# Performance work log

Hardware: AMD Instinct MI355X
Metric: run time of the kernel (lower is better)

## Reference

```python
import jax, jax.numpy as jnp
import numpy as np

N_OSC = 60
B = 65536
DT = 0.1
STEPS = 10
PHI_INV = 2.0 / (1.0 + np.sqrt(5.0))


def setup_inputs() -> dict:
    key = jax.random.key(0)
    k1, k2, k3 = jax.random.split(key, 3)
    theta = jax.random.uniform(k1, (B, N_OSC), dtype=jnp.float32) * (2.0 * np.pi) - np.pi
    K = jax.random.normal(k2, (N_OSC, N_OSC), dtype=jnp.float32) * 0.1
    omega = jax.random.normal(k3, (N_OSC,), dtype=jnp.float32) * 0.1
    return {
        'theta': theta,
        'K': K,
        'omega': omega,
        'K_global': jnp.float32(PHI_INV),
        'coupling_mod': jnp.float32(0.6),        # phase_coupling['quasi_crystal']
        'neg_entropy_gate': jnp.float32(0.5),
        'critical_slow_factor': jnp.float32(0.1),
        'delta_s_neg': jnp.float32(0.8),          # NegativeEntropyState constant
        'relaxation_time': jnp.float32(5.0),      # NegativeEntropyState constant
    }


def reference(theta, K, omega, K_global, coupling_mod, neg_entropy_gate,
              critical_slow_factor, delta_s_neg, relaxation_time):
    n = theta.shape[-1]
    K_eff = K * coupling_mod                               # [n, n]
    critical_factor = 1.0 / (1.0 + critical_slow_factor * relaxation_time)
    eff_dt = DT * critical_factor
    boost = 1.0 + neg_entropy_gate * delta_s_neg
    scale = K_global * boost / n

    def step(th, _):
        # theta_diff[b, i, j] = th[b, j] - th[b, i]
        diff = th[..., None, :] - th[..., :, None]          # [B, n, n]
        coupling_sum = jnp.sum(K_eff * jnp.sin(diff), axis=-1)  # [B, n]
        th = th + eff_dt * (omega + scale * coupling_sum)
        th = jnp.arctan2(jnp.sin(th), jnp.cos(th))          # wrap to (-pi, pi]
        return th, None

    theta, _ = jax.lax.scan(step, theta, None, length=STEPS)
    cos_m = jnp.cos(theta).mean(axis=-1)
    sin_m = jnp.sin(theta).mean(axis=-1)
    coherence = jnp.sqrt(cos_m ** 2 + sin_m ** 2)           # [B]
    return theta, coherence
```

## Files before the change

kernel.cpp:

```cpp
#include <hip/hip_runtime.h>
#include <stdint.h>
#include <math.h>


#define B_TOTAL 65536
#define NOSC 60
#define STEPS 10

using short8  = __attribute__((ext_vector_type(8))) short;
using floatx4 = __attribute__((ext_vector_type(4))) float;

#if __has_builtin(__builtin_amdgcn_perm)
__device__ __forceinline__ unsigned int perm_b32(unsigned int s0, unsigned int s1, unsigned int sel) {
    return __builtin_amdgcn_perm(s0, s1, sel);
}
#else
__device__ __forceinline__ unsigned int perm_b32(unsigned int s0, unsigned int s1, unsigned int sel) {
    unsigned long long pool = ((unsigned long long)s0 << 32) | s1;
    unsigned int r = 0;
#pragma unroll
    for (int b = 0; b < 4; ++b) {
        unsigned int s = (sel >> (8 * b)) & 0xff;
        r |= ((unsigned int)((pool >> (8 * s)) & 0xff)) << (8 * b);
    }
    return r;
}
#endif

__device__ __forceinline__ unsigned int fbits(float x)   { return __builtin_bit_cast(unsigned int, x); }
__device__ __forceinline__ float        bitsf(unsigned int u) { return __builtin_bit_cast(float, u); }

__global__ __launch_bounds__(64, 2)
void kuramoto_kernel(const float* __restrict__ theta_in,
                     const float* __restrict__ Kmat,
                     const float* __restrict__ omega,
                     const float* __restrict__ p_kglobal,
                     const float* __restrict__ p_cmod,
                     const float* __restrict__ p_gate,
                     const float* __restrict__ p_slow,
                     const float* __restrict__ p_dsneg,
                     const float* __restrict__ p_relax,
                     float* __restrict__ theta_out,
                     float* __restrict__ coh_out)
{
    __shared__ uint64_t tile[16 * 66];

    const int lane = threadIdx.x & 63;
    const int lidx = lane & 15;
    const int quad = lane >> 4;

    const float kglobal = p_kglobal[0];
    const float cmod    = p_cmod[0];
    const float gate    = p_gate[0];
    const float slow    = p_slow[0];
    const float dsneg   = p_dsneg[0];
    const float relax   = p_relax[0];

    float eff_dt, scale;
    {
#pragma clang fp contract(off)
        const float a     = slow * relax;
        const float b     = 1.0f + a;
        const float crit  = 1.0f / b;
        eff_dt            = 0.1f * crit;
        const float boost = 1.0f + gate * dsneg;
        scale             = (kglobal * boost) / 60.0f;
    }

    const int batch0 = blockIdx.x * 16;

    short8 KH[4][2], KL[4][2];
#pragma unroll
    for (int nt = 0; nt < 4; ++nt) {
        const int n = nt * 16 + lidx;
        const bool okn = (n < NOSC);
#pragma unroll
        for (int kt = 0; kt < 2; ++kt) {
            const int k0 = kt * 32 + quad * 8;
            float kv[8];
            if (okn && (k0 + 7) < NOSC) {
                const float4* rp = (const float4*)(Kmat + n * NOSC + k0);
                const float4 a = rp[0], b = rp[1];
                kv[0]=a.x; kv[1]=a.y; kv[2]=a.z; kv[3]=a.w;
                kv[4]=b.x; kv[5]=b.y; kv[6]=b.z; kv[7]=b.w;
            } else {
#pragma unroll
                for (int j = 0; j < 8; ++j)
                    kv[j] = (okn && (k0 + j) < NOSC) ? Kmat[n * NOSC + k0 + j] : 0.0f;
            }
#pragma unroll
            for (int j = 0; j < 8; ++j) {
                const float v = kv[j] * cmod;
                const unsigned int hb = fbits(v) & 0xffff0000u;
                const float rlo = v - bitsf(hb);
                KH[nt][kt][j] = (short)(hb >> 16);
                KL[nt][kt][j] = (short)(fbits(rlo) >> 16);
            }
        }
    }

    float th[4][4], sn[4][4], cn[4][4];
    float omg[4];
#pragma unroll
    for (int nt = 0; nt < 4; ++nt) {
        const int i = nt * 16 + lidx;
        omg[nt] = (i < NOSC) ? omega[i] : 0.0f;
#pragma unroll
        for (int r = 0; r < 4; ++r) {
            const int b = batch0 + quad * 4 + r;
            th[nt][r] = (i < NOSC) ? theta_in[b * NOSC + i] : 0.0f;
            __sincosf(th[nt][r], &sn[nt][r], &cn[nt][r]);
        }
    }

    const float PI_F = 3.14159274101257324f;
    const float C_HI = 6.28318548202514648f;
    const float C_LO = -1.7484556e-7f;

    for (int t = 0; t < STEPS; ++t) {
#pragma unroll
        for (int nt = 0; nt < 4; ++nt) {
#pragma unroll
            for (int r = 0; r < 4; ++r) {
                const float s = sn[nt][r], c = cn[nt][r];
                const unsigned int us = fbits(s);
                const float rs = s - bitsf(us & 0xffff0000u);
                const unsigned int uc = fbits(c);
                const float rc = c - bitsf(uc & 0xffff0000u);
                const unsigned int w0 = perm_b32(fbits(rs), us, 0x07060302u);
                const unsigned int w1 = perm_b32(fbits(rc), uc, 0x07060302u);
                tile[(quad * 4 + r) * 66 + nt * 16 + lidx] =
                    (uint64_t)w0 | ((uint64_t)w1 << 32);
            }
        }
        __syncthreads();

        floatx4 accS[4], accC[4];
#pragma unroll
        for (int nt = 0; nt < 4; ++nt) { accS[nt] = (floatx4)0.0f; accC[nt] = (floatx4)0.0f; }
#pragma unroll
        for (int kt = 0; kt < 2; ++kt) {
            const uint4* p = (const uint4*)(tile + lidx * 66 + kt * 32 + quad * 8);
            uint4 q[4];
            q[0] = p[0]; q[1] = p[1]; q[2] = p[2]; q[3] = p[3];
            union U { short8 v; unsigned int u[4]; };
            U ash, asl, ach, acl;
#pragma unroll
            for (int pr = 0; pr < 4; ++pr) {
                ash.u[pr] = perm_b32(q[pr].z, q[pr].x, 0x05040100u);
                asl.u[pr] = perm_b32(q[pr].z, q[pr].x, 0x07060302u);
                ach.u[pr] = perm_b32(q[pr].w, q[pr].y, 0x05040100u);
                acl.u[pr] = perm_b32(q[pr].w, q[pr].y, 0x07060302u);
            }
#pragma unroll
            for (int nt = 0; nt < 4; ++nt) {
                accS[nt] = __builtin_amdgcn_mfma_f32_16x16x32_bf16(ash.v, KH[nt][kt], accS[nt], 0, 0, 0);
                accS[nt] = __builtin_amdgcn_mfma_f32_16x16x32_bf16(asl.v, KH[nt][kt], accS[nt], 0, 0, 0);
                accS[nt] = __builtin_amdgcn_mfma_f32_16x16x32_bf16(ash.v, KL[nt][kt], accS[nt], 0, 0, 0);
                accC[nt] = __builtin_amdgcn_mfma_f32_16x16x32_bf16(ach.v, KH[nt][kt], accC[nt], 0, 0, 0);
                accC[nt] = __builtin_amdgcn_mfma_f32_16x16x32_bf16(acl.v, KH[nt][kt], accC[nt], 0, 0, 0);
                accC[nt] = __builtin_amdgcn_mfma_f32_16x16x32_bf16(ach.v, KL[nt][kt], accC[nt], 0, 0, 0);
            }
        }

#pragma unroll
        for (int nt = 0; nt < 4; ++nt) {
#pragma unroll
            for (int r = 0; r < 4; ++r) {
                const float S = accS[nt][r];
                const float C = accC[nt][r];
                const float coup = cn[nt][r] * S - sn[nt][r] * C;
                float nth;
                {
#pragma clang fp contract(off)
                    const float t1 = scale * coup;
                    const float t2 = omg[nt] + t1;
                    const float t3 = eff_dt * t2;
                    nth = th[nt][r] + t3;
                }
                float n = 0.0f;
                n = (nth >=  PI_F) ?  1.0f : n;
                n = (nth <= -PI_F) ? -1.0f : n;
                float y = fmaf(n, -C_HI, nth);
                y = fmaf(n, -C_LO, y);
                th[nt][r] = y;
                __sincosf(y, &sn[nt][r], &cn[nt][r]);
            }
        }
    }

#pragma unroll
    for (int nt = 0; nt < 4; ++nt) {
        const int i = nt * 16 + lidx;
        if (i < NOSC) {
#pragma unroll
            for (int r = 0; r < 4; ++r) {
                const int b = batch0 + quad * 4 + r;
                theta_out[b * NOSC + i] = th[nt][r];
            }
        }
    }

    float pc[4], ps[4];
#pragma unroll
    for (int r = 0; r < 4; ++r) { pc[r] = 0.0f; ps[r] = 0.0f; }
#pragma unroll
    for (int nt = 0; nt < 4; ++nt) {
        const int i = nt * 16 + lidx;
        const bool ok = (i < NOSC);
#pragma unroll
        for (int r = 0; r < 4; ++r) {
            pc[r] += ok ? cn[nt][r] : 0.0f;
            ps[r] += ok ? sn[nt][r] : 0.0f;
        }
    }
#pragma unroll
    for (int mask = 1; mask < 16; mask <<= 1) {
#pragma unroll
        for (int r = 0; r < 4; ++r) {
            pc[r] += __shfl_xor(pc[r], mask, 16);
            ps[r] += __shfl_xor(ps[r], mask, 16);
        }
    }
    if (lidx == 0) {
#pragma unroll
        for (int r = 0; r < 4; ++r) {
            const float cm = pc[r] / 60.0f;
            const float sm = ps[r] / 60.0f;
            coh_out[batch0 + quad * 4 + r] = sqrtf(cm * cm + sm * sm);
        }
    }
}

extern "C" void kernel_launch(void* const* d_in, const int* in_sizes, int n_in,
                              void* d_out, int out_size, void* d_ws, size_t ws_size,
                              hipStream_t stream) {
    const float* theta = (const float*)d_in[0];
    const float* Kmat  = (const float*)d_in[1];
    const float* omg   = (const float*)d_in[2];
    const float* kg    = (const float*)d_in[3];
    const float* cmod  = (const float*)d_in[4];
    const float* gate  = (const float*)d_in[5];
    const float* slow  = (const float*)d_in[6];
    const float* dsn   = (const float*)d_in[7];
    const float* relax = (const float*)d_in[8];
    float* out = (float*)d_out;

    kuramoto_kernel<<<dim3(B_TOTAL / 16), dim3(64), 0, stream>>>(
        theta, Kmat, omg, kg, cmod, gate, slow, dsn, relax,
        out, out + (size_t)B_TOTAL * NOSC);
}
```

Measured before the change: 123.3 us.

## Transpose MFMA formulation to keep phase state in registers, removing LDS staging

```diff
diff --git a/kernel.cpp b/kernel.cpp
--- a/kernel.cpp
+++ b/kernel.cpp
@@ -7,7 +7,7 @@
 #define NOSC 60
 #define STEPS 10
 
-using short8  = __attribute__((ext_vector_type(8))) short;
+using short4v = __attribute__((ext_vector_type(4))) short;
 using floatx4 = __attribute__((ext_vector_type(4))) float;
 
 #if __has_builtin(__builtin_amdgcn_perm)
@@ -27,8 +27,23 @@
 }
 #endif
 
-__device__ __forceinline__ unsigned int fbits(float x)   { return __builtin_bit_cast(unsigned int, x); }
+__device__ __forceinline__ unsigned int fbits(float x)        { return __builtin_bit_cast(unsigned int, x); }
 __device__ __forceinline__ float        bitsf(unsigned int u) { return __builtin_bit_cast(float, u); }
+
+#if __has_builtin(__builtin_amdgcn_mfma_f32_16x16x16bf16_1k)
+__device__ __forceinline__ floatx4 mfma16(short4v a, short4v b, floatx4 c) {
+    return __builtin_amdgcn_mfma_f32_16x16x16bf16_1k(a, b, c, 0, 0, 0);
+}
+#else
+__device__ __forceinline__ floatx4 mfma16(short4v a, short4v b, floatx4 c) {
+    asm("v_mfma_f32_16x16x16_bf16 %0, %1, %2, %0" : "+v"(c) : "v"(a), "v"(b));
+    return c;
+}
+#endif
+
+__device__ __forceinline__ unsigned int pack_hi_pair(float a, float b) {
+    return perm_b32(fbits(b), fbits(a), 0x07060302u);
+}
 
 __global__ __launch_bounds__(64, 2)
 void kuramoto_kernel(const float* __restrict__ theta_in,
@@ -43,8 +58,6 @@
                      float* __restrict__ theta_out,
                      float* __restrict__ coh_out)
 {
-    __shared__ uint64_t tile[16 * 66];
-
     const int lane = threadIdx.x & 63;
     const int lidx = lane & 15;
     const int quad = lane >> 4;
@@ -68,49 +81,55 @@
     }
 
     const int batch0 = blockIdx.x * 16;
-
-    short8 KH[4][2], KL[4][2];
-#pragma unroll
-    for (int nt = 0; nt < 4; ++nt) {
-        const int n = nt * 16 + lidx;
-        const bool okn = (n < NOSC);
-#pragma unroll
-        for (int kt = 0; kt < 2; ++kt) {
-            const int k0 = kt * 32 + quad * 8;
-            float kv[8];
-            if (okn && (k0 + 7) < NOSC) {
-                const float4* rp = (const float4*)(Kmat + n * NOSC + k0);
-                const float4 a = rp[0], b = rp[1];
-                kv[0]=a.x; kv[1]=a.y; kv[2]=a.z; kv[3]=a.w;
-                kv[4]=b.x; kv[5]=b.y; kv[6]=b.z; kv[7]=b.w;
+    const int brow   = (batch0 + lidx) * NOSC;
+
+    short4v AH[4][4], AL[4][4];
+#pragma unroll
+    for (int nt = 0; nt < 4; ++nt) {
+        const int i = nt * 16 + lidx;
+        const bool okn = (i < NOSC);
+#pragma unroll
+        for (int kt = 0; kt < 4; ++kt) {
+            const int k0 = kt * 16 + quad * 4;
+            float kv[4];
+            if (okn && (k0 + 3) < NOSC) {
+                const float4 a = *(const float4*)(Kmat + i * NOSC + k0);
+                kv[0] = a.x; kv[1] = a.y; kv[2] = a.z; kv[3] = a.w;
             } else {
 #pragma unroll
-                for (int j = 0; j < 8; ++j)
-                    kv[j] = (okn && (k0 + j) < NOSC) ? Kmat[n * NOSC + k0 + j] : 0.0f;
-            }
-#pragma unroll
-            for (int j = 0; j < 8; ++j) {
+                for (int j = 0; j < 4; ++j)
+                    kv[j] = (okn && (k0 + j) < NOSC) ? Kmat[i * NOSC + k0 + j] : 0.0f;
+            }
+            short4v h, l;
+#pragma unroll
+            for (int j = 0; j < 4; ++j) {
                 const float v = kv[j] * cmod;
                 const unsigned int hb = fbits(v) & 0xffff0000u;
                 const float rlo = v - bitsf(hb);
-                KH[nt][kt][j] = (short)(hb >> 16);
-                KL[nt][kt][j] = (short)(fbits(rlo) >> 16);
-            }
-        }
-    }
-
-    float th[4][4], sn[4][4], cn[4][4];
-    float omg[4];
-#pragma unroll
-    for (int nt = 0; nt < 4; ++nt) {
-        const int i = nt * 16 + lidx;
-        omg[nt] = (i < NOSC) ? omega[i] : 0.0f;
-#pragma unroll
-        for (int r = 0; r < 4; ++r) {
-            const int b = batch0 + quad * 4 + r;
-            th[nt][r] = (i < NOSC) ? theta_in[b * NOSC + i] : 0.0f;
+                h[j] = (short)(hb >> 16);
+                l[j] = (short)(fbits(rlo) >> 16);
+            }
+            AH[nt][kt] = h;
+            AL[nt][kt] = l;
+        }
+    }
+
+    float th[4][4], sn[4][4], cn[4][4], omg[4][4];
+#pragma unroll
+    for (int nt = 0; nt < 4; ++nt) {
+        const int o0 = nt * 16 + quad * 4;
+        if (o0 + 3 < NOSC) {
+            const float4 tv = *(const float4*)(theta_in + brow + o0);
+            const float4 ov = *(const float4*)(omega + o0);
+            th[nt][0] = tv.x; th[nt][1] = tv.y; th[nt][2] = tv.z; th[nt][3] = tv.w;
+            omg[nt][0] = ov.x; omg[nt][1] = ov.y; omg[nt][2] = ov.z; omg[nt][3] = ov.w;
+        } else {
+#pragma unroll
+            for (int r = 0; r < 4; ++r) { th[nt][r] = 0.0f; omg[nt][r] = 0.0f; }
+        }
+#pragma unroll
+        for (int r = 0; r < 4; ++r)
             __sincosf(th[nt][r], &sn[nt][r], &cn[nt][r]);
-        }
     }
 
     const float PI_F = 3.14159274101257324f;
@@ -118,48 +137,39 @@
     const float C_LO = -1.7484556e-7f;
 
     for (int t = 0; t < STEPS; ++t) {
-#pragma unroll
-        for (int nt = 0; nt < 4; ++nt) {
+        floatx4 accS[4], accC[4];
+#pragma unroll
+        for (int nt = 0; nt < 4; ++nt) { accS[nt] = (floatx4)0.0f; accC[nt] = (floatx4)0.0f; }
+
+#pragma unroll
+        for (int kt = 0; kt < 4; ++kt) {
+            union PU { unsigned int u[2]; short4v v; };
+            PU bsh, bsl, bch, bcl;
+            float sl[4], cl[4];
 #pragma unroll
             for (int r = 0; r < 4; ++r) {
-                const float s = sn[nt][r], c = cn[nt][r];
-                const unsigned int us = fbits(s);
-                const float rs = s - bitsf(us & 0xffff0000u);
-                const unsigned int uc = fbits(c);
-                const float rc = c - bitsf(uc & 0xffff0000u);
-                const unsigned int w0 = perm_b32(fbits(rs), us, 0x07060302u);
-                const unsigned int w1 = perm_b32(fbits(rc), uc, 0x07060302u);
-                tile[(quad * 4 + r) * 66 + nt * 16 + lidx] =
-                    (uint64_t)w0 | ((uint64_t)w1 << 32);
-            }
-        }
-        __syncthreads();
-
-        floatx4 accS[4], accC[4];
-#pragma unroll
-        for (int nt = 0; nt < 4; ++nt) { accS[nt] = (floatx4)0.0f; accC[nt] = (floatx4)0.0f; }
-#pragma unroll
-        for (int kt = 0; kt < 2; ++kt) {
-            const uint4* p = (const uint4*)(tile + lidx * 66 + kt * 32 + quad * 8);
-            uint4 q[4];
-            q[0] = p[0]; q[1] = p[1]; q[2] = p[2]; q[3] = p[3];
-            union U { short8 v; unsigned int u[4]; };
-            U ash, asl, ach, acl;
-#pragma unroll
-            for (int pr = 0; pr < 4; ++pr) {
-                ash.u[pr] = perm_b32(q[pr].z, q[pr].x, 0x05040100u);
-                asl.u[pr] = perm_b32(q[pr].z, q[pr].x, 0x07060302u);
-                ach.u[pr] = perm_b32(q[pr].w, q[pr].y, 0x05040100u);
-                acl.u[pr] = perm_b32(q[pr].w, q[pr].y, 0x07060302u);
-            }
+                const unsigned int us = fbits(sn[kt][r]);
+                sl[r] = sn[kt][r] - bitsf(us & 0xffff0000u);
+                const unsigned int uc = fbits(cn[kt][r]);
+                cl[r] = cn[kt][r] - bitsf(uc & 0xffff0000u);
+            }
+            bsh.u[0] = pack_hi_pair(sn[kt][0], sn[kt][1]);
+            bsh.u[1] = pack_hi_pair(sn[kt][2], sn[kt][3]);
+            bsl.u[0] = pack_hi_pair(sl[0], sl[1]);
+            bsl.u[1] = pack_hi_pair(sl[2], sl[3]);
+            bch.u[0] = pack_hi_pair(cn[kt][0], cn[kt][1]);
+            bch.u[1] = pack_hi_pair(cn[kt][2], cn[kt][3]);
+            bcl.u[0] = pack_hi_pair(cl[0], cl[1]);
+            bcl.u[1] = pack_hi_pair(cl[2], cl[3]);
+
 #pragma unroll
             for (int nt = 0; nt < 4; ++nt) {
-                accS[nt] = __builtin_amdgcn_mfma_f32_16x16x32_bf16(ash.v, KH[nt][kt], accS[nt], 0, 0, 0);
-                accS[nt] = __builtin_amdgcn_mfma_f32_16x16x32_bf16(asl.v, KH[nt][kt], accS[nt], 0, 0, 0);
-                accS[nt] = __builtin_amdgcn_mfma_f32_16x16x32_bf16(ash.v, KL[nt][kt], accS[nt], 0, 0, 0);
-                accC[nt] = __builtin_amdgcn_mfma_f32_16x16x32_bf16(ach.v, KH[nt][kt], accC[nt], 0, 0, 0);
-                accC[nt] = __builtin_amdgcn_mfma_f32_16x16x32_bf16(acl.v, KH[nt][kt], accC[nt], 0, 0, 0);
-                accC[nt] = __builtin_amdgcn_mfma_f32_16x16x32_bf16(ach.v, KL[nt][kt], accC[nt], 0, 0, 0);
+                accS[nt] = mfma16(AH[nt][kt], bsh.v, accS[nt]);
+                accS[nt] = mfma16(AL[nt][kt], bsh.v, accS[nt]);
+                accS[nt] = mfma16(AH[nt][kt], bsl.v, accS[nt]);
+                accC[nt] = mfma16(AH[nt][kt], bch.v, accC[nt]);
+                accC[nt] = mfma16(AL[nt][kt], bch.v, accC[nt]);
+                accC[nt] = mfma16(AH[nt][kt], bcl.v, accC[nt]);
             }
         }
 
@@ -174,7 +184,7 @@
                 {
 #pragma clang fp contract(off)
                     const float t1 = scale * coup;
-                    const float t2 = omg[nt] + t1;
+                    const float t2 = omg[nt][r] + t1;
                     const float t3 = eff_dt * t2;
                     nth = th[nt][r] + t3;
                 }
@@ -191,44 +201,30 @@
 
 #pragma unroll
     for (int nt = 0; nt < 4; ++nt) {
-        const int i = nt * 16 + lidx;
-        if (i < NOSC) {
-#pragma unroll
-            for (int r = 0; r < 4; ++r) {
-                const int b = batch0 + quad * 4 + r;
-                theta_out[b * NOSC + i] = th[nt][r];
-            }
-        }
-    }
-
-    float pc[4], ps[4];
-#pragma unroll
-    for (int r = 0; r < 4; ++r) { pc[r] = 0.0f; ps[r] = 0.0f; }
-#pragma unroll
-    for (int nt = 0; nt < 4; ++nt) {
-        const int i = nt * 16 + lidx;
-        const bool ok = (i < NOSC);
-#pragma unroll
-        for (int r = 0; r < 4; ++r) {
-            pc[r] += ok ? cn[nt][r] : 0.0f;
-            ps[r] += ok ? sn[nt][r] : 0.0f;
-        }
-    }
-#pragma unroll
-    for (int mask = 1; mask < 16; mask <<= 1) {
-#pragma unroll
-        for (int r = 0; r < 4; ++r) {
-            pc[r] += __shfl_xor(pc[r], mask, 16);
-            ps[r] += __shfl_xor(ps[r], mask, 16);
-        }
-    }
-    if (lidx == 0) {
-#pragma unroll
-        for (int r = 0; r < 4; ++r) {
-            const float cm = pc[r] / 60.0f;
-            const float sm = ps[r] / 60.0f;
-            coh_out[batch0 + quad * 4 + r] = sqrtf(cm * cm + sm * sm);
-        }
+        const int o0 = nt * 16 + quad * 4;
+        if (o0 + 3 < NOSC) {
+            float4 tv;
+            tv.x = th[nt][0]; tv.y = th[nt][1]; tv.z = th[nt][2]; tv.w = th[nt][3];
+            *(float4*)(theta_out + brow + o0) = tv;
+        }
+    }
+
+    float pc = 0.0f, ps = 0.0f;
+#pragma unroll
+    for (int nt = 0; nt < 4; ++nt) {
+        if (nt * 16 + quad * 4 < NOSC) {
+#pragma unroll
+            for (int r = 0; r < 4; ++r) { pc += cn[nt][r]; ps += sn[nt][r]; }
+        }
+    }
+    pc += __shfl_xor(pc, 16);
+    ps += __shfl_xor(ps, 16);
+    pc += __shfl_xor(pc, 32);
+    ps += __shfl_xor(ps, 32);
+    if (quad == 0) {
+        const float cm = pc / 60.0f;
+        const float sm = ps / 60.0f;
+        coh_out[batch0 + lidx] = sqrtf(cm * cm + sm * sm);
     }
 }
 
```

Result: no change. 125.3 us (+1.6%).
